# Performance work log

Measured on AMD Instinct MI355X. Metric: run time of the kernel, lower is better.

## Reference

```python
import jax, jax.numpy as jnp
import numpy as np

DK = 64  # embedding_size / h = 1024 / 16


def setup_inputs() -> dict:
    key = jax.random.key(0)
    k1, k2, k3 = jax.random.split(key, 3)
    S = 8192
    return {
        "q": jax.random.normal(k1, (S, DK), dtype=jnp.float32),
        "k": jax.random.normal(k2, (S, DK), dtype=jnp.float32),
        "v": jax.random.normal(k3, (S, DK), dtype=jnp.float32),
    }


def reference(q, k, v):
    # scores: [S, S]; NOTE: source scales by 1/dk (not 1/sqrt(dk)) — kept faithful.
    qk = jnp.matmul(q, k.T) * (1.0 / DK)
    S = qk.shape[0]
    # causal mask: position (i, j) allowed iff i >= j (0 added), else -inf
    i = jnp.arange(S)[:, None]
    j = jnp.arange(S)[None, :]
    qk = jnp.where(i >= j, qk, -jnp.inf)
    attn = jax.nn.softmax(qk, axis=-1)
    return jnp.matmul(attn, v)
```

## Files before the change

kernel.cpp:

```cpp
#include <hip/hip_runtime.h>
#include <hip/hip_bf16.h>

#define S_LEN 8192
#define DKD   64
#define BM    64
#define BN    64
#define PAD   8
#define LDK   (DKD + PAD)

#define CHUNK 512
#define NC    (S_LEN / CHUNK)
#define NWORK 1088

#define WS_NEED ((size_t)2 * S_LEN * DKD * 2 + (size_t)NC * S_LEN * 4 + (size_t)NC * S_LEN * DKD * 2)

typedef __bf16 bf16x8 __attribute__((ext_vector_type(8)));
typedef float  f32x4  __attribute__((ext_vector_type(4)));
typedef unsigned short ushort8v __attribute__((ext_vector_type(8)));
typedef unsigned short ushort4v __attribute__((ext_vector_type(4)));

typedef __attribute__((address_space(3))) unsigned int lds_uint;
typedef const __attribute__((address_space(1))) unsigned int glb_uint;

__device__ __forceinline__ unsigned short f2bf(float f) {
  union { float f; unsigned u; } v; v.f = f;
  unsigned u = v.u;
  return (unsigned short)((u + 0x7fffu + ((u >> 16) & 1u)) >> 16);
}
__device__ __forceinline__ float bf2f(unsigned short s) {
  union { unsigned u; float f; } v; v.u = ((unsigned)s) << 16;
  return v.f;
}
__device__ __forceinline__ unsigned pk2(float a, float b) {
  union { float f; unsigned u; } x, y; x.f = a; y.f = b;
  return ((x.u + 0x8000u) >> 16) | ((y.u + 0x8000u) & 0xffff0000u);
}
__device__ __forceinline__ bf16x8 q_frag8(const float* p, float sc) {
  float4 u = *(const float4*)p;
  float4 w = *(const float4*)(p + 4);
  union { ushort8v s; bf16x8 b; } r;
  r.s[0] = f2bf(u.x * sc); r.s[1] = f2bf(u.y * sc);
  r.s[2] = f2bf(u.z * sc); r.s[3] = f2bf(u.w * sc);
  r.s[4] = f2bf(w.x * sc); r.s[5] = f2bf(w.y * sc);
  r.s[6] = f2bf(w.z * sc); r.s[7] = f2bf(w.w * sc);
  return r.b;
}

__global__ __launch_bounds__(256) void precompute(const float* __restrict__ k,
                                                  const float* __restrict__ v,
                                                  unsigned short* __restrict__ Ff) {
  __shared__ unsigned short Ls[64][72];
  const int b = blockIdx.x, tid = threadIdx.x;
  unsigned short* tb = Ff + ((size_t)b << 13);

#pragma unroll
  for (int j = 0; j < 4; ++j) {
    int vi = tid + j * 256;
    int row = vi >> 4, c4 = vi & 15;
    float4 x = *(const float4*)(v + ((size_t)(b * 64 + row)) * DKD + c4 * 4);
    Ls[row][c4 * 4 + 0] = f2bf(x.x);
    Ls[row][c4 * 4 + 1] = f2bf(x.y);
    Ls[row][c4 * 4 + 2] = f2bf(x.z);
    Ls[row][c4 * 4 + 3] = f2bf(x.w);
  }

#pragma unroll
  for (int j = 0; j < 2; ++j) {
    int idx = tid + j * 256;
    int f = idx >> 6, lane = idx & 63;
    int col = lane & 15, quad = lane >> 4;
    int t = f >> 1, c = f & 1;
    const float* src = k + ((size_t)(b * 64 + 16 * t + col)) * DKD + c * 32 + quad * 8;
    union { ushort8v s; bf16x8 bb; } r;
    r.bb = q_frag8(src, 1.0f);
    *(ushort8v*)(tb + (size_t)(f * 64 + lane) * 8) = r.s;
  }
  __syncthreads();

#pragma unroll
  for (int j = 0; j < 2; ++j) {
    int idx = tid + j * 256;
    int f8 = idx >> 6, lane = idx & 63;
    int col = lane & 15, quad = lane >> 4;
    int dt = f8 >> 1, c = f8 & 1;
    int d = 16 * dt + col;
    ushort8v o;
#pragma unroll
    for (int j2 = 0; j2 < 8; ++j2) {
      int kk = c * 32 + quad * 8 + j2;
      int s = (((kk & 7) >> 2) + 2 * (kk >> 5)) * 16 + (((kk >> 3) & 3) << 2) + (kk & 3);
      o[j2] = Ls[s][d];
    }
    *(ushort8v*)(tb + (size_t)((8 + f8) * 64 + lane) * 8) = o;
  }
}

__device__ __forceinline__ void stage_tile(const unsigned short* tb,
                                           unsigned short* dst,
                                           int wave) {
#pragma unroll
  for (int p = 0; p < 4; ++p) {
    const int seg = p * 4 + wave;
    __builtin_amdgcn_global_load_lds(
        (glb_uint*)(tb + ((size_t)seg << 9) + (size_t)(threadIdx.x & 63) * 8),
        (lds_uint*)(dst + ((size_t)seg << 9)),
        16, 0, 0);
  }
}

__global__ __launch_bounds__(256) void attn_partial(const float* __restrict__ qg,
                                                    const unsigned short* __restrict__ Ff,
                                                    unsigned short* __restrict__ Opart,
                                                    float* __restrict__ l_ws) {
  const int wr = (NWORK - 1) - blockIdx.x;
  int g = (int)((sqrtf((float)wr + 1.0f) - 1.0f) * 0.5f);
  while (4 * (g + 1) * (g + 2) <= wr) ++g;
  while (4 * g * (g + 1) > wr) --g;
  const int r0  = wr - 4 * g * (g + 1);
  const int qq  = r0 / (g + 1);
  const int qt  = 8 * g + qq;
  const int cch = r0 - qq * (g + 1);

  const int q0 = qt * BM, chunk0 = cch * CHUNK;
  const int n_kt = min(CHUNK / BN, qt - 8 * cch + 1);
  const int tile0 = cch * 8;

  __shared__ __align__(16) unsigned short Buf[2][8192];

  const int tid = threadIdx.x, wave = tid >> 6, lane = tid & 63;
  const int col = lane & 15, quad = lane >> 4;

  const int qidx = q0 + wave * 16 + col;
  const float* qp = qg + (size_t)qidx * DKD;
  bf16x8 b0 = q_frag8(qp + quad * 8, 1.0f / 64.0f);
  bf16x8 b1 = q_frag8(qp + 32 + quad * 8, 1.0f / 64.0f);

  float lsum = 0.0f;
  f32x4 Of[4];
#pragma unroll
  for (int i = 0; i < 4; ++i) Of[i] = f32x4{0.0f, 0.0f, 0.0f, 0.0f};

  stage_tile(Ff + ((size_t)tile0 << 13), &Buf[0][0], wave);
  __syncthreads();

  for (int it = 0; it < n_kt; ++it) {
    if (it + 1 < n_kt)
      stage_tile(Ff + ((size_t)(tile0 + it + 1) << 13), &Buf[(it + 1) & 1][0], wave);

    const unsigned short* B = &Buf[it & 1][0];
    const int k0 = chunk0 + it * BN;

    bf16x8 kf[8];
#pragma unroll
    for (int f = 0; f < 8; ++f)
      kf[f] = *(const bf16x8*)(B + (size_t)((f << 6) + lane) * 8);

    f32x4 Sf[4];
#pragma unroll
    for (int t = 0; t < 4; ++t) {
      f32x4 acc = f32x4{0.0f, 0.0f, 0.0f, 0.0f};
      acc = __builtin_amdgcn_mfma_f32_16x16x32_bf16(kf[2 * t], b0, acc, 0, 0, 0);
      acc = __builtin_amdgcn_mfma_f32_16x16x32_bf16(kf[2 * t + 1], b1, acc, 0, 0, 0);
      Sf[t] = acc;
    }

    bf16x8 vf[8];
#pragma unroll
    for (int f = 0; f < 8; ++f)
      vf[f] = *(const bf16x8*)(B + (size_t)(((8 + f) << 6) + lane) * 8);

#pragma unroll
    for (int t = 0; t < 4; ++t) {
      int kb = k0 + t * 16 + quad * 4;
#pragma unroll
      for (int r = 0; r < 4; ++r) {
        float p = __expf(Sf[t][r]);
        p = (kb + r <= qidx) ? p : 0.0f;
        Sf[t][r] = p;
        lsum += p;
      }
    }

    union { unsigned u[4]; bf16x8 b; } pa0, pa1;
    pa0.u[0] = pk2(Sf[0][0], Sf[0][1]); pa0.u[1] = pk2(Sf[0][2], Sf[0][3]);
    pa0.u[2] = pk2(Sf[1][0], Sf[1][1]); pa0.u[3] = pk2(Sf[1][2], Sf[1][3]);
    pa1.u[0] = pk2(Sf[2][0], Sf[2][1]); pa1.u[1] = pk2(Sf[2][2], Sf[2][3]);
    pa1.u[2] = pk2(Sf[3][0], Sf[3][1]); pa1.u[3] = pk2(Sf[3][2], Sf[3][3]);

#pragma unroll
    for (int dt = 0; dt < 4; ++dt) {
      Of[dt] = __builtin_amdgcn_mfma_f32_16x16x32_bf16(pa0.b, vf[2 * dt], Of[dt], 0, 0, 0);
      Of[dt] = __builtin_amdgcn_mfma_f32_16x16x32_bf16(pa1.b, vf[2 * dt + 1], Of[dt], 0, 0, 0);
    }

    __syncthreads();
  }

  lsum += __shfl_xor(lsum, 16);
  lsum += __shfl_xor(lsum, 32);
  if (lane < 16)
    l_ws[cch * S_LEN + q0 + wave * 16 + lane] = lsum;

#pragma unroll
  for (int r = 0; r < 4; ++r) {
    int rowg = q0 + wave * 16 + quad * 4 + r;
    uint2 o2;
    o2.x = pk2(Of[0][r], Of[1][r]);
    o2.y = pk2(Of[2][r], Of[3][r]);
    *(uint2*)(Opart + ((size_t)cch * S_LEN + rowg) * DKD + col * 4) = o2;
  }
}

__global__ __launch_bounds__(256) void attn_merge(const unsigned short* __restrict__ Opart,
                                                  const float* __restrict__ l_ws,
                                                  float* __restrict__ out) {
  int idx = blockIdx.x * 256 + threadIdx.x;
  int row = idx >> 3, m = idx & 7;
  int nc = (row >> 9) + 1;

  float acc[8] = {0, 0, 0, 0, 0, 0, 0, 0};
  float L = 0.0f;
  for (int c = 0; c < nc; ++c) {
    L += l_ws[c * S_LEN + row];
    ushort8v o = *(const ushort8v*)(Opart + ((size_t)c * S_LEN + row) * DKD + m * 8);
#pragma unroll
    for (int j = 0; j < 8; ++j) acc[j] += bf2f(o[j]);
  }
  float inv = 1.0f / L;
#pragma unroll
  for (int j0 = 0; j0 < 4; ++j0) {
    float2 w2 = { acc[j0] * inv, acc[j0 + 4] * inv };
    *(float2*)(out + (size_t)row * DKD + 16 * j0 + 2 * m) = w2;
  }
}

__global__ __launch_bounds__(128) void attn_fwd(const float* __restrict__ qg,
                                                const float* __restrict__ kg,
                                                const float* __restrict__ vg,
                                                float* __restrict__ out) {
  __shared__ __align__(16) unsigned short Qs[32][LDK];
  __shared__ __align__(16) unsigned short Ksh[BN][LDK];
  __shared__ __align__(16) unsigned short Vt[DKD][LDK];
  __shared__ __align__(16) unsigned short Ps[2][16][LDK];

  const int tid = threadIdx.x, wave = tid >> 6, lane = tid & 63;
  const int col = lane & 15, quad = lane >> 4;
  const int q0 = blockIdx.x * 32;

#pragma unroll
  for (int r = 0; r < 4; ++r) {
    int vi = tid + r * 128;
    int row = vi >> 4, c4 = vi & 15;
    if (row < 32) {
      float4 val = *(const float4*)(qg + (size_t)(q0 + row) * DKD + c4 * 4);
      Qs[row][c4 * 4 + 0] = f2bf(val.x);
      Qs[row][c4 * 4 + 1] = f2bf(val.y);
      Qs[row][c4 * 4 + 2] = f2bf(val.z);
      Qs[row][c4 * 4 + 3] = f2bf(val.w);
    }
  }

  float m_run[4], l_run[4];
  f32x4 Of[4];
#pragma unroll
  for (int i = 0; i < 4; ++i) {
    m_run[i] = -1e30f; l_run[i] = 0.0f;
    Of[i] = f32x4{0.0f, 0.0f, 0.0f, 0.0f};
  }

  const int n_tiles = (q0 + 31) / BN + 1;
  for (int it = 0; it < n_tiles; ++it) {
    __syncthreads();
    const int k0 = it * BN;
#pragma unroll
    for (int r = 0; r < 8; ++r) {
      int vi = tid + r * 128;
      int row = vi >> 4, c4 = vi & 15;
      float4 kv = *(const float4*)(kg + (size_t)(k0 + row) * DKD + c4 * 4);
      Ksh[row][c4 * 4 + 0] = f2bf(kv.x);
      Ksh[row][c4 * 4 + 1] = f2bf(kv.y);
      Ksh[row][c4 * 4 + 2] = f2bf(kv.z);
      Ksh[row][c4 * 4 + 3] = f2bf(kv.w);
      float4 vv = *(const float4*)(vg + (size_t)(k0 + row) * DKD + c4 * 4);
      Vt[c4 * 4 + 0][row] = f2bf(vv.x);
      Vt[c4 * 4 + 1][row] = f2bf(vv.y);
      Vt[c4 * 4 + 2][row] = f2bf(vv.z);
      Vt[c4 * 4 + 3][row] = f2bf(vv.w);
    }
    __syncthreads();

    f32x4 Sf[4];
    const unsigned short* qrow = &Qs[wave * 16 + col][0];
#pragma unroll
    for (int t = 0; t < 4; ++t) {
      f32x4 acc = f32x4{0.0f, 0.0f, 0.0f, 0.0f};
#pragma unroll
      for (int c = 0; c < 2; ++c) {
        bf16x8 a = *(const bf16x8*)(qrow + c * 32 + quad * 8);
        bf16x8 b = *(const bf16x8*)(&Ksh[t * 16 + col][c * 32 + quad * 8]);
        acc = __builtin_amdgcn_mfma_f32_16x16x32_bf16(a, b, acc, 0, 0, 0);
      }
      Sf[t] = acc;
    }

    const float scale = 1.0f / 64.0f;
    float rmax[4] = {-1e30f, -1e30f, -1e30f, -1e30f};
#pragma unroll
    for (int t = 0; t < 4; ++t) {
      int kidx = k0 + t * 16 + col;
#pragma unroll
      for (int r = 0; r < 4; ++r) {
        int qidx = q0 + wave * 16 + quad * 4 + r;
        float s = Sf[t][r] * scale;
        s = (kidx <= qidx) ? s : -1e30f;
        Sf[t][r] = s;
        rmax[r] = fmaxf(rmax[r], s);
      }
    }
#pragma unroll
    for (int off = 1; off <= 8; off <<= 1)
#pragma unroll
      for (int r = 0; r < 4; ++r)
        rmax[r] = fmaxf(rmax[r], __shfl_xor(rmax[r], off));

    float alpha[4], rsum[4];
#pragma unroll
    for (int r = 0; r < 4; ++r) {
      float mn = fmaxf(m_run[r], rmax[r]);
      alpha[r] = __expf(m_run[r] - mn);
      m_run[r] = mn;
      rsum[r] = 0.0f;
    }
#pragma unroll
    for (int t = 0; t < 4; ++t)
#pragma unroll
      for (int r = 0; r < 4; ++r) {
        float p = __expf(Sf[t][r] - m_run[r]);
        Sf[t][r] = p;
        rsum[r] += p;
      }
#pragma unroll
    for (int off = 1; off <= 8; off <<= 1)
#pragma unroll
      for (int r = 0; r < 4; ++r)
        rsum[r] += __shfl_xor(rsum[r], off);
#pragma unroll
    for (int r = 0; r < 4; ++r)
      l_run[r] = l_run[r] * alpha[r] + rsum[r];
#pragma unroll
    for (int dt = 0; dt < 4; ++dt)
#pragma unroll
      for (int r = 0; r < 4; ++r)
        Of[dt][r] *= alpha[r];

#pragma unroll
    for (int t = 0; t < 4; ++t)
#pragma unroll
      for (int r = 0; r < 4; ++r)
        Ps[wave][quad * 4 + r][t * 16 + col] = f2bf(Sf[t][r]);
    __syncthreads();

    const unsigned short* prow = &Ps[wave][col][0];
#pragma unroll
    for (int dt = 0; dt < 4; ++dt) {
#pragma unroll
      for (int c = 0; c < 2; ++c) {
        bf16x8 a = *(const bf16x8*)(prow + c * 32 + quad * 8);
        bf16x8 b = *(const bf16x8*)(&Vt[dt * 16 + col][c * 32 + quad * 8]);
        Of[dt] = __builtin_amdgcn_mfma_f32_16x16x32_bf16(a, b, Of[dt], 0, 0, 0);
      }
    }
  }

#pragma unroll
  for (int r = 0; r < 4; ++r) {
    float inv = 1.0f / l_run[r];
    int qrow_g = q0 + wave * 16 + quad * 4 + r;
#pragma unroll
    for (int dt = 0; dt < 4; ++dt)
      out[(size_t)qrow_g * DKD + dt * 16 + col] = Of[dt][r] * inv;
  }
}

extern "C" void kernel_launch(void* const* d_in, const int* in_sizes, int n_in,
                              void* d_out, int out_size, void* d_ws, size_t ws_size,
                              hipStream_t stream) {
  const float* q = (const float*)d_in[0];
  const float* k = (const float*)d_in[1];
  const float* v = (const float*)d_in[2];
  float* out = (float*)d_out;

  if (ws_size >= WS_NEED) {
    unsigned short* Ff    = (unsigned short*)d_ws;
    float* l_ws           = (float*)(Ff + (size_t)2 * S_LEN * DKD);
    unsigned short* Opart = (unsigned short*)(l_ws + (size_t)NC * S_LEN);

    hipLaunchKernelGGL(precompute, dim3(S_LEN / 64), dim3(256), 0, stream, k, v, Ff);
    hipLaunchKernelGGL(attn_partial, dim3(NWORK), dim3(256), 0, stream,
                       q, Ff, Opart, l_ws);
    hipLaunchKernelGGL(attn_merge, dim3(S_LEN * 8 / 256), dim3(256), 0, stream,
                       Opart, l_ws, out);
  } else {
    hipLaunchKernelGGL(attn_fwd, dim3(S_LEN / 32), dim3(128), 0, stream, q, k, v, out);
  }
}
```

Before: 88.24 us.

## Process two 64-row query subtiles per block to reuse staged K/V tiles

Doubles the query tile to 128 rows per block. Each wave now computes two 16-row query groups against the same K/V fragments loaded from LDS, which halves K/V staging traffic and the block count. The triangular work mapping is rewritten for the new tile shape, and launch bounds request two blocks per CU. The cost is higher register pressure from the doubled accumulators, and fewer, coarser blocks on the diagonal that may do more masked-out work.

```diff
diff --git a/kernel.cpp b/kernel.cpp
--- a/kernel.cpp
+++ b/kernel.cpp
@@ -3,14 +3,14 @@
 
 #define S_LEN 8192
 #define DKD   64
-#define BM    64
+#define BM    128
 #define BN    64
 #define PAD   8
 #define LDK   (DKD + PAD)
 
 #define CHUNK 512
 #define NC    (S_LEN / CHUNK)
-#define NWORK 1088
+#define NWORK 544
 
 #define WS_NEED ((size_t)2 * S_LEN * DKD * 2 + (size_t)NC * S_LEN * 4 + (size_t)NC * S_LEN * DKD * 2)
 
@@ -108,21 +108,21 @@
   }
 }
 
-__global__ __launch_bounds__(256) void attn_partial(const float* __restrict__ qg,
-                                                    const unsigned short* __restrict__ Ff,
-                                                    unsigned short* __restrict__ Opart,
-                                                    float* __restrict__ l_ws) {
+__global__ __launch_bounds__(256, 2) void attn_partial(const float* __restrict__ qg,
+                                                       const unsigned short* __restrict__ Ff,
+                                                       unsigned short* __restrict__ Opart,
+                                                       float* __restrict__ l_ws) {
   const int wr = (NWORK - 1) - blockIdx.x;
-  int g = (int)((sqrtf((float)wr + 1.0f) - 1.0f) * 0.5f);
-  while (4 * (g + 1) * (g + 2) <= wr) ++g;
-  while (4 * g * (g + 1) > wr) --g;
-  const int r0  = wr - 4 * g * (g + 1);
+  int g = (int)((sqrtf((float)(2 * wr) + 1.0f) - 1.0f) * 0.5f);
+  while (2 * (g + 1) * (g + 2) <= wr) ++g;
+  while (2 * g * (g + 1) > wr) --g;
+  const int r0  = wr - 2 * g * (g + 1);
   const int qq  = r0 / (g + 1);
-  const int qt  = 8 * g + qq;
+  const int qt  = 4 * g + qq;
   const int cch = r0 - qq * (g + 1);
 
   const int q0 = qt * BM, chunk0 = cch * CHUNK;
-  const int n_kt = min(CHUNK / BN, qt - 8 * cch + 1);
+  const int n_kt = min(CHUNK / BN, 2 * (qt - 4 * cch) + 2);
   const int tile0 = cch * 8;
 
   __shared__ __align__(16) unsigned short Buf[2][8192];
@@ -130,15 +130,22 @@
   const int tid = threadIdx.x, wave = tid >> 6, lane = tid & 63;
   const int col = lane & 15, quad = lane >> 4;
 
-  const int qidx = q0 + wave * 16 + col;
-  const float* qp = qg + (size_t)qidx * DKD;
-  bf16x8 b0 = q_frag8(qp + quad * 8, 1.0f / 64.0f);
-  bf16x8 b1 = q_frag8(qp + 32 + quad * 8, 1.0f / 64.0f);
-
-  float lsum = 0.0f;
-  f32x4 Of[4];
-#pragma unroll
-  for (int i = 0; i < 4; ++i) Of[i] = f32x4{0.0f, 0.0f, 0.0f, 0.0f};
+  const int qidxA = q0 + wave * 16 + col;
+  const int qidxB = qidxA + 64;
+  const float* qpA = qg + (size_t)qidxA * DKD;
+  const float* qpB = qg + (size_t)qidxB * DKD;
+  bf16x8 a0 = q_frag8(qpA + quad * 8, 1.0f / 64.0f);
+  bf16x8 a1 = q_frag8(qpA + 32 + quad * 8, 1.0f / 64.0f);
+  bf16x8 c0 = q_frag8(qpB + quad * 8, 1.0f / 64.0f);
+  bf16x8 c1 = q_frag8(qpB + 32 + quad * 8, 1.0f / 64.0f);
+
+  float lsumA = 0.0f, lsumB = 0.0f;
+  f32x4 OfA[4], OfB[4];
+#pragma unroll
+  for (int i = 0; i < 4; ++i) {
+    OfA[i] = f32x4{0.0f, 0.0f, 0.0f, 0.0f};
+    OfB[i] = f32x4{0.0f, 0.0f, 0.0f, 0.0f};
+  }
 
   stage_tile(Ff + ((size_t)tile0 << 13), &Buf[0][0], wave);
   __syncthreads();
@@ -155,13 +162,20 @@
     for (int f = 0; f < 8; ++f)
       kf[f] = *(const bf16x8*)(B + (size_t)((f << 6) + lane) * 8);
 
-    f32x4 Sf[4];
+    f32x4 SA[4], SB[4];
 #pragma unroll
     for (int t = 0; t < 4; ++t) {
       f32x4 acc = f32x4{0.0f, 0.0f, 0.0f, 0.0f};
-      acc = __builtin_amdgcn_mfma_f32_16x16x32_bf16(kf[2 * t], b0, acc, 0, 0, 0);
-      acc = __builtin_amdgcn_mfma_f32_16x16x32_bf16(kf[2 * t + 1], b1, acc, 0, 0, 0);
-      Sf[t] = acc;
+      acc = __builtin_amdgcn_mfma_f32_16x16x32_bf16(kf[2 * t], a0, acc, 0, 0, 0);
+      acc = __builtin_amdgcn_mfma_f32_16x16x32_bf16(kf[2 * t + 1], a1, acc, 0, 0, 0);
+      SA[t] = acc;
+    }
+#pragma unroll
+    for (int t = 0; t < 4; ++t) {
+      f32x4 acc = f32x4{0.0f, 0.0f, 0.0f, 0.0f};
+      acc = __builtin_amdgcn_mfma_f32_16x16x32_bf16(kf[2 * t], c0, acc, 0, 0, 0);
+      acc = __builtin_amdgcn_mfma_f32_16x16x32_bf16(kf[2 * t + 1], c1, acc, 0, 0, 0);
+      SB[t] = acc;
     }
 
     bf16x8 vf[8];
@@ -174,40 +188,61 @@
       int kb = k0 + t * 16 + quad * 4;
 #pragma unroll
       for (int r = 0; r < 4; ++r) {
-        float p = __expf(Sf[t][r]);
-        p = (kb + r <= qidx) ? p : 0.0f;
-        Sf[t][r] = p;
-        lsum += p;
+        float pA = __expf(SA[t][r]);
+        pA = (kb + r <= qidxA) ? pA : 0.0f;
+        SA[t][r] = pA;
+        lsumA += pA;
+        float pB = __expf(SB[t][r]);
+        pB = (kb + r <= qidxB) ? pB : 0.0f;
+        SB[t][r] = pB;
+        lsumB += pB;
       }
     }
 
-    union { unsigned u[4]; bf16x8 b; } pa0, pa1;
-    pa0.u[0] = pk2(Sf[0][0], Sf[0][1]); pa0.u[1] = pk2(Sf[0][2], Sf[0][3]);
-    pa0.u[2] = pk2(Sf[1][0], Sf[1][1]); pa0.u[3] = pk2(Sf[1][2], Sf[1][3]);
-    pa1.u[0] = pk2(Sf[2][0], Sf[2][1]); pa1.u[1] = pk2(Sf[2][2], Sf[2][3]);
-    pa1.u[2] = pk2(Sf[3][0], Sf[3][1]); pa1.u[3] = pk2(Sf[3][2], Sf[3][3]);
+    union { unsigned u[4]; bf16x8 b; } pa0, pa1, pb0, pb1;
+    pa0.u[0] = pk2(SA[0][0], SA[0][1]); pa0.u[1] = pk2(SA[0][2], SA[0][3]);
+    pa0.u[2] = pk2(SA[1][0], SA[1][1]); pa0.u[3] = pk2(SA[1][2], SA[1][3]);
+    pa1.u[0] = pk2(SA[2][0], SA[2][1]); pa1.u[1] = pk2(SA[2][2], SA[2][3]);
+    pa1.u[2] = pk2(SA[3][0], SA[3][1]); pa1.u[3] = pk2(SA[3][2], SA[3][3]);
+    pb0.u[0] = pk2(SB[0][0], SB[0][1]); pb0.u[1] = pk2(SB[0][2], SB[0][3]);
+    pb0.u[2] = pk2(SB[1][0], SB[1][1]); pb0.u[3] = pk2(SB[1][2], SB[1][3]);
+    pb1.u[0] = pk2(SB[2][0], SB[2][1]); pb1.u[1] = pk2(SB[2][2], SB[2][3]);
+    pb1.u[2] = pk2(SB[3][0], SB[3][1]); pb1.u[3] = pk2(SB[3][2], SB[3][3]);
 
 #pragma unroll
     for (int dt = 0; dt < 4; ++dt) {
-      Of[dt] = __builtin_amdgcn_mfma_f32_16x16x32_bf16(pa0.b, vf[2 * dt], Of[dt], 0, 0, 0);
-      Of[dt] = __builtin_amdgcn_mfma_f32_16x16x32_bf16(pa1.b, vf[2 * dt + 1], Of[dt], 0, 0, 0);
+      OfA[dt] = __builtin_amdgcn_mfma_f32_16x16x32_bf16(pa0.b, vf[2 * dt], OfA[dt], 0, 0, 0);
+      OfA[dt] = __builtin_amdgcn_mfma_f32_16x16x32_bf16(pa1.b, vf[2 * dt + 1], OfA[dt], 0, 0, 0);
+    }
+#pragma unroll
+    for (int dt = 0; dt < 4; ++dt) {
+      OfB[dt] = __builtin_amdgcn_mfma_f32_16x16x32_bf16(pb0.b, vf[2 * dt], OfB[dt], 0, 0, 0);
+      OfB[dt] = __builtin_amdgcn_mfma_f32_16x16x32_bf16(pb1.b, vf[2 * dt + 1], OfB[dt], 0, 0, 0);
     }
 
     __syncthreads();
   }
 
-  lsum += __shfl_xor(lsum, 16);
-  lsum += __shfl_xor(lsum, 32);
-  if (lane < 16)
-    l_ws[cch * S_LEN + q0 + wave * 16 + lane] = lsum;
+  lsumA += __shfl_xor(lsumA, 16);
+  lsumA += __shfl_xor(lsumA, 32);
+  lsumB += __shfl_xor(lsumB, 16);
+  lsumB += __shfl_xor(lsumB, 32);
+  if (lane < 16) {
+    l_ws[cch * S_LEN + q0 + wave * 16 + lane] = lsumA;
+    l_ws[cch * S_LEN + q0 + 64 + wave * 16 + lane] = lsumB;
+  }
 
 #pragma unroll
   for (int r = 0; r < 4; ++r) {
-    int rowg = q0 + wave * 16 + quad * 4 + r;
-    uint2 o2;
-    o2.x = pk2(Of[0][r], Of[1][r]);
-    o2.y = pk2(Of[2][r], Of[3][r]);
-    *(uint2*)(Opart + ((size_t)cch * S_LEN + rowg) * DKD + col * 4) = o2;
+    int rowgA = q0 + wave * 16 + quad * 4 + r;
+    uint2 oA;
+    oA.x = pk2(OfA[0][r], OfA[1][r]);
+    oA.y = pk2(OfA[2][r], OfA[3][r]);
+    *(uint2*)(Opart + ((size_t)cch * S_LEN + rowgA) * DKD + col * 4) = oA;
+    uint2 oB;
+    oB.x = pk2(OfB[0][r], OfB[1][r]);
+    oB.y = pk2(OfB[2][r], OfB[3][r]);
+    *(uint2*)(Opart + ((size_t)cch * S_LEN + rowgA + 64) * DKD + col * 4) = oB;
   }
 }
 
```

New measurement: 89.95 us. Within noise of the previous version (+1.9%).
